# Kernel optimization log

Hardware: AMD Instinct MI355X
Metric: run time of the kernel (lower is better)

Reference implementation:

```python
import jax, jax.numpy as jnp
import numpy as np

NUM_PINS = 10_000_000
NUM_NETS = 2_500_000


def setup_inputs() -> dict:
    key = jax.random.key(0)
    k1, k2, k3 = jax.random.split(key, 3)
    pos = jax.random.normal(k1, (2 * NUM_PINS,), dtype=jnp.float32)
    pin2net_map = jax.random.randint(k2, (NUM_PINS,), 0, NUM_NETS).astype(jnp.int32)
    net_weights = jax.random.uniform(k3, (NUM_NETS,), dtype=jnp.float32)
    net_mask = jnp.ones((NUM_NETS,), dtype=bool)
    pin_mask = jnp.zeros((NUM_PINS,), dtype=bool)
    inv_gamma = jnp.ones((1,), dtype=jnp.float32)
    return {"pos": pos, "pin2net_map": pin2net_map, "net_weights": net_weights,
            "net_mask": net_mask, "pin_mask": pin_mask, "inv_gamma": inv_gamma}


def _wawl(pos, pin2net_map, net_weights, net_mask, inv_gamma, num_nets):
    # pos = concat(x, y); reshape to [P, 2] so segment ops handle x,y together
    P = pos.shape[0] // 2
    xy = pos.reshape(2, P).T  # [P, 2]
    ig = inv_gamma[0]

    # per-net max/min for numerical stability (shift cancels in the ratio)
    seg_max = jax.lax.stop_gradient(
        jax.ops.segment_max(xy, pin2net_map, num_segments=num_nets))  # [N,2]
    seg_min = jax.lax.stop_gradient(
        jax.ops.segment_min(xy, pin2net_map, num_segments=num_nets))  # [N,2]

    ex = jnp.exp((xy - seg_max[pin2net_map]) * ig)   # [P,2]
    enx = jnp.exp((seg_min[pin2net_map] - xy) * ig)  # [P,2]

    sum_ex = jax.ops.segment_sum(ex, pin2net_map, num_segments=num_nets)
    sum_enx = jax.ops.segment_sum(enx, pin2net_map, num_segments=num_nets)
    sum_xex = jax.ops.segment_sum(xy * ex, pin2net_map, num_segments=num_nets)
    sum_xenx = jax.ops.segment_sum(xy * enx, pin2net_map, num_segments=num_nets)

    # guard empty nets (sum == 0) to avoid 0/0
    valid = sum_ex > 0
    wl_pos = jnp.where(valid, sum_xex / jnp.where(valid, sum_ex, 1.0), 0.0)
    wl_neg = jnp.where(valid, sum_xenx / jnp.where(valid, sum_enx, 1.0), 0.0)
    wl_net = wl_pos - wl_neg  # [N,2]

    w = jnp.where(net_mask, net_weights, 0.0)  # [N]
    return jnp.sum(wl_net * w[:, None])


def reference(pos, pin2net_map, net_weights, net_mask, pin_mask, inv_gamma):
    num_nets = net_weights.shape[0]
    return _wawl(pos, pin2net_map, net_weights, net_mask, inv_gamma, num_nets)
```

## Files before the change

### kernel.cpp

```cpp
#include <hip/hip_runtime.h>
#include <hip/hip_fp16.h>


#define NPB      2048
#define NPB_LOG  11
#define CAP      9216
#define NBMAX    2048
#define CHUNK    16384
#define TB       1024

__global__ void init_kernel(int* __restrict__ alloc, int NB, float* __restrict__ out) {
    int i = blockIdx.x * blockDim.x + threadIdx.x;
    if (i == 0) out[0] = 0.f;
    if (i < NB) alloc[i] = i * CAP;
}

__global__ __launch_bounds__(TB)
void bucket_kernel(const int* __restrict__ p2n, const float* __restrict__ pos, int P,
                   int* __restrict__ alloc, uint2* __restrict__ rec) {
    __shared__ int   hist_delta[NBMAX];
    __shared__ int   cur[NBMAX];
    __shared__ uint2 stage[CHUNK];
    __shared__ unsigned wtot[TB / 64];

    const int tid  = threadIdx.x;
    const int lane = tid & 63;
    const int wid  = tid >> 6;
    const int start = blockIdx.x * CHUNK;
    const int cnt_chunk = min(CHUNK, P - start);

    hist_delta[2 * tid]     = 0;
    hist_delta[2 * tid + 1] = 0;
    __syncthreads();

#pragma unroll
    for (int k = 0; k < CHUNK / TB; ++k) {
        int i = start + k * TB + tid;
        if (i < P) atomicAdd(&hist_delta[p2n[i] >> NPB_LOG], 1);
    }
    __syncthreads();

    unsigned e0 = (unsigned)hist_delta[2 * tid];
    unsigned e1 = (unsigned)hist_delta[2 * tid + 1];
    unsigned pair = e0 + e1;
    unsigned inc = pair;
#pragma unroll
    for (int d = 1; d < 64; d <<= 1) {
        unsigned u = (unsigned)__shfl_up((int)inc, d, 64);
        if (lane >= d) inc += u;
    }
    if (lane == 63) wtot[wid] = inc;
    __syncthreads();
    unsigned wbase = 0;
    for (int k = 0; k < wid; ++k) wbase += wtot[k];
    unsigned off0 = wbase + inc - pair;
    unsigned off1 = off0 + e0;
    int b0 = 2 * tid, b1 = b0 + 1;
    int g0 = e0 ? atomicAdd(&alloc[b0], (int)e0) : 0;
    int g1 = e1 ? atomicAdd(&alloc[b1], (int)e1) : 0;
    hist_delta[b0] = g0 - (int)off0;
    hist_delta[b1] = g1 - (int)off1;
    cur[b0] = (int)off0;
    cur[b1] = (int)off1;
    __syncthreads();

#pragma unroll
    for (int k = 0; k < CHUNK / TB; ++k) {
        int i = start + k * TB + tid;
        if (i < P) {
            int n = p2n[i];
            __half2 h = __floats2half2_rn(pos[i], pos[P + i]);
            uint2 r;
            r.x = *reinterpret_cast<unsigned*>(&h);
            r.y = (unsigned)n;
            int p = atomicAdd(&cur[n >> NPB_LOG], 1);
            stage[p] = r;
        }
    }
    __syncthreads();

#pragma unroll
    for (int k = 0; k < CHUNK / TB; ++k) {
        int slot = k * TB + tid;
        if (slot < cnt_chunk) {
            uint2 r = stage[slot];
            int b = (int)(r.y >> NPB_LOG);
            int addr = hist_delta[b] + slot;
            if (addr < (b + 1) * CAP)
                rec[addr] = r;
        }
    }
}

__global__ __launch_bounds__(TB)
void reduce_kernel(const uint2* __restrict__ rec, const int* __restrict__ alloc,
                   const float* __restrict__ w, const void* __restrict__ mask,
                   const float* __restrict__ inv_gamma, int N, float* __restrict__ out) {
    __shared__ unsigned       head[NPB];
    __shared__ unsigned       spin[CAP];
    __shared__ unsigned short nxt[CAP];
    __shared__ float          wsum[TB / 64];

    const int tid  = threadIdx.x;
    const int lane = tid & 63;
    const int wid  = tid >> 6;
    const int b    = blockIdx.x;
    const int base = b * CAP;

    int count = alloc[b] - base;
    if (count > CAP) count = CAP;
    const float ig = inv_gamma[0];

    head[2 * tid]     = 0xFFFFu;
    head[2 * tid + 1] = 0xFFFFu;
    __syncthreads();

    for (int e = tid; e < count; e += TB) {
        uint2 r = rec[base + e];
        spin[e] = r.x;
        unsigned old = atomicExch(&head[r.y & (NPB - 1)], (unsigned)e);
        nxt[e] = (unsigned short)old;
    }
    __syncthreads();

    const bool mask_is_byte = (((const unsigned*)mask)[0] == 0x01010101u);
    float local = 0.f;
#pragma unroll
    for (int rep = 0; rep < 2; ++rep) {
        int j = tid + rep * TB;
        int n = (b << NPB_LOG) + j;
        if (n >= N) continue;
        unsigned p = head[j];
        if (p != 0xFFFFu) {
            float sex = 0.f, sxex = 0.f, senx = 0.f, sxenx = 0.f;
            float sey = 0.f, syey = 0.f, seny = 0.f, syeny = 0.f;
            while (p != 0xFFFFu) {
                unsigned u = spin[p];
                __half2 h = *reinterpret_cast<__half2*>(&u);
                float x = __low2float(h), y = __high2float(h);
                float ex  = __expf(x * ig);
                float enx = __expf(-x * ig);
                float ey  = __expf(y * ig);
                float eny = __expf(-y * ig);
                sex += ex;  sxex += x * ex;  senx += enx;  sxenx += x * enx;
                sey += ey;  syey += y * ey;  seny += eny;  syeny += y * eny;
                p = nxt[p];
            }
            float val = sxex / sex - sxenx / senx + syey / sey - syeny / seny;
            bool m = mask_is_byte ? (((const unsigned char*)mask)[n] != 0)
                                  : (((const int*)mask)[n] != 0);
            local += val * (m ? w[n] : 0.f);
        }
    }

#pragma unroll
    for (int o = 32; o > 0; o >>= 1) local += __shfl_down(local, o, 64);
    if (lane == 0) wsum[wid] = local;
    __syncthreads();
    if (tid == 0) {
        float s = 0.f;
        for (int k = 0; k < TB / 64; ++k) s += wsum[k];
        atomicAdd(out, s);
    }
}

extern "C" void kernel_launch(void* const* d_in, const int* in_sizes, int n_in,
                              void* d_out, int out_size, void* d_ws, size_t ws_size,
                              hipStream_t stream) {
    const float* pos       = (const float*)d_in[0];
    const int*   p2n       = (const int*)d_in[1];
    const float* wts       = (const float*)d_in[2];
    const void*  net_mask  = d_in[3];
    const float* inv_gamma = (const float*)d_in[5];

    int P = in_sizes[0] / 2;
    int N = in_sizes[2];
    int NB = (N + NPB - 1) >> NPB_LOG;
    if (NB > NBMAX) return;

    int*   alloc = (int*)d_ws;
    uint2* rec   = (uint2*)((char*)d_ws + NBMAX * sizeof(int));
    float* out   = (float*)d_out;

    int chunks = (P + CHUNK - 1) / CHUNK;

    hipLaunchKernelGGL(init_kernel,   dim3((NBMAX + 255) / 256), dim3(256), 0, stream,
                       alloc, NB, out);
    hipLaunchKernelGGL(bucket_kernel, dim3(chunks),              dim3(TB),  0, stream,
                       p2n, pos, P, alloc, rec);
    hipLaunchKernelGGL(reduce_kernel, dim3(NB),                  dim3(TB),  0, stream,
                       rec, alloc, wts, net_mask, inv_gamma, N, out);
}
```

Before: 293.5 us.

## Replace global atomic bucket allocation with per-chunk sorted segments and offset metadata

The bucket kernel now builds per-bucket linked lists in shared memory and writes each chunk's records sorted by bucket into its own chunk region, storing per-bucket offsets in a metadata table. This removes the global atomicAdd allocator. The reduce kernel prefix-scans those offsets to gather each bucket's records from every chunk. The per-thread serial list walks in the bucket kernel make the global writes uncoalesced. In the reduce kernel each thread copies a variable-length segment serially, which can cause load imbalance and scattered reads.

```diff
diff --git a/kernel.cpp b/kernel.cpp
--- a/kernel.cpp
+++ b/kernel.cpp
@@ -4,45 +4,60 @@
 
 #define NPB      2048
 #define NPB_LOG  11
-#define CAP      9216
-#define NBMAX    2048
-#define CHUNK    16384
+#define CHUNK    8192
+#define CAPB     9216
 #define TB       1024
 
-__global__ void init_kernel(int* __restrict__ alloc, int NB, float* __restrict__ out) {
-    int i = blockIdx.x * blockDim.x + threadIdx.x;
-    if (i == 0) out[0] = 0.f;
-    if (i < NB) alloc[i] = i * CAP;
+__global__ void init_kernel(float* __restrict__ out) {
+    if (threadIdx.x == 0 && blockIdx.x == 0) out[0] = 0.f;
 }
 
 __global__ __launch_bounds__(TB)
-void bucket_kernel(const int* __restrict__ p2n, const float* __restrict__ pos, int P,
-                   int* __restrict__ alloc, uint2* __restrict__ rec) {
-    __shared__ int   hist_delta[NBMAX];
-    __shared__ int   cur[NBMAX];
-    __shared__ uint2 stage[CHUNK];
+void bucket_kernel(const int* __restrict__ p2n, const float* __restrict__ pos,
+                   int P, int C, int NB,
+                   uint2* __restrict__ rec, int* __restrict__ offmeta) {
+    __shared__ unsigned head[NPB];
+    __shared__ uint2    elem[CHUNK];
     __shared__ unsigned wtot[TB / 64];
 
     const int tid  = threadIdx.x;
     const int lane = tid & 63;
     const int wid  = tid >> 6;
-    const int start = blockIdx.x * CHUNK;
+    const int c     = blockIdx.x;
+    const int start = c * CHUNK;
     const int cnt_chunk = min(CHUNK, P - start);
 
-    hist_delta[2 * tid]     = 0;
-    hist_delta[2 * tid + 1] = 0;
+    head[2 * tid]     = 0xFFFFu;
+    head[2 * tid + 1] = 0xFFFFu;
     __syncthreads();
 
 #pragma unroll
     for (int k = 0; k < CHUNK / TB; ++k) {
-        int i = start + k * TB + tid;
-        if (i < P) atomicAdd(&hist_delta[p2n[i] >> NPB_LOG], 1);
-    }
-    __syncthreads();
-
-    unsigned e0 = (unsigned)hist_delta[2 * tid];
-    unsigned e1 = (unsigned)hist_delta[2 * tid + 1];
-    unsigned pair = e0 + e1;
+        int e = k * TB + tid;
+        int i = start + e;
+        if (i < P) {
+            int n = p2n[i];
+            __half2 h = __floats2half2_rn(pos[i], pos[P + i]);
+            unsigned coords = *reinterpret_cast<unsigned*>(&h);
+            unsigned old = atomicExch(&head[n >> NPB_LOG], (unsigned)e);
+            elem[e] = make_uint2(coords,
+                                 ((unsigned)(n & (NPB - 1)) << 16) | (old & 0xFFFFu));
+        }
+    }
+    __syncthreads();
+
+    const int b0 = 2 * tid, b1 = 2 * tid + 1;
+    unsigned cnt0 = 0, cnt1 = 0;
+    if (b0 < NB) {
+        unsigned p = head[b0];
+        while (p != 0xFFFFu) { cnt0++; p = elem[p].y & 0xFFFFu; }
+    }
+    if (b1 < NB) {
+        unsigned p = head[b1];
+        while (p != 0xFFFFu) { cnt1++; p = elem[p].y & 0xFFFFu; }
+    }
+
+    unsigned pair = cnt0 + cnt1;
     unsigned inc = pair;
 #pragma unroll
     for (int d = 1; d < 64; d <<= 1) {
@@ -53,73 +68,94 @@
     __syncthreads();
     unsigned wbase = 0;
     for (int k = 0; k < wid; ++k) wbase += wtot[k];
-    unsigned off0 = wbase + inc - pair;
-    unsigned off1 = off0 + e0;
-    int b0 = 2 * tid, b1 = b0 + 1;
-    int g0 = e0 ? atomicAdd(&alloc[b0], (int)e0) : 0;
-    int g1 = e1 ? atomicAdd(&alloc[b1], (int)e1) : 0;
-    hist_delta[b0] = g0 - (int)off0;
-    hist_delta[b1] = g1 - (int)off1;
-    cur[b0] = (int)off0;
-    cur[b1] = (int)off1;
-    __syncthreads();
-
-#pragma unroll
-    for (int k = 0; k < CHUNK / TB; ++k) {
-        int i = start + k * TB + tid;
-        if (i < P) {
-            int n = p2n[i];
-            __half2 h = __floats2half2_rn(pos[i], pos[P + i]);
-            uint2 r;
-            r.x = *reinterpret_cast<unsigned*>(&h);
-            r.y = (unsigned)n;
-            int p = atomicAdd(&cur[n >> NPB_LOG], 1);
-            stage[p] = r;
-        }
-    }
-    __syncthreads();
-
-#pragma unroll
-    for (int k = 0; k < CHUNK / TB; ++k) {
-        int slot = k * TB + tid;
-        if (slot < cnt_chunk) {
-            uint2 r = stage[slot];
-            int b = (int)(r.y >> NPB_LOG);
-            int addr = hist_delta[b] + slot;
-            if (addr < (b + 1) * CAP)
-                rec[addr] = r;
+    const unsigned off0 = wbase + inc - pair;
+    const unsigned off1 = off0 + cnt0;
+
+    if (b0 < NB) offmeta[(size_t)b0 * C + c] = (int)off0;
+    if (b1 < NB) offmeta[(size_t)b1 * C + c] = (int)off1;
+    if (tid == 0) offmeta[(size_t)NB * C + c] = cnt_chunk;
+
+    if (b0 < NB) {
+        unsigned p = head[b0], k = 0;
+        while (p != 0xFFFFu) {
+            uint2 el = elem[p];
+            rec[(size_t)start + off0 + k] = make_uint2(el.x, el.y >> 16);
+            k++;
+            p = el.y & 0xFFFFu;
+        }
+    }
+    if (b1 < NB) {
+        unsigned p = head[b1], k = 0;
+        while (p != 0xFFFFu) {
+            uint2 el = elem[p];
+            rec[(size_t)start + off1 + k] = make_uint2(el.x, el.y >> 16);
+            k++;
+            p = el.y & 0xFFFFu;
         }
     }
 }
 
 __global__ __launch_bounds__(TB)
-void reduce_kernel(const uint2* __restrict__ rec, const int* __restrict__ alloc,
+void reduce_kernel(const uint2* __restrict__ rec, const int* __restrict__ offmeta,
                    const float* __restrict__ w, const void* __restrict__ mask,
-                   const float* __restrict__ inv_gamma, int N, float* __restrict__ out) {
+                   const float* __restrict__ inv_gamma, int N, int C, int NB,
+                   float* __restrict__ out) {
     __shared__ unsigned       head[NPB];
-    __shared__ unsigned       spin[CAP];
-    __shared__ unsigned short nxt[CAP];
-    __shared__ float          wsum[TB / 64];
+    __shared__ unsigned       spin[CAPB];
+    __shared__ unsigned short nxt[CAPB];
+    __shared__ int            sA[CHUNK / 4];
+    __shared__ int            dA[CHUNK / 4];
+    __shared__ unsigned wtot[TB / 64];
+    __shared__ float    wsum[TB / 64];
 
     const int tid  = threadIdx.x;
     const int lane = tid & 63;
     const int wid  = tid >> 6;
     const int b    = blockIdx.x;
-    const int base = b * CAP;
-
-    int count = alloc[b] - base;
-    if (count > CAP) count = CAP;
     const float ig = inv_gamma[0];
 
     head[2 * tid]     = 0xFFFFu;
     head[2 * tid + 1] = 0xFFFFu;
-    __syncthreads();
-
-    for (int e = tid; e < count; e += TB) {
-        uint2 r = rec[base + e];
-        spin[e] = r.x;
-        unsigned old = atomicExch(&head[r.y & (NPB - 1)], (unsigned)e);
-        nxt[e] = (unsigned short)old;
+    for (int c = tid; c < C; c += TB) {
+        int s = offmeta[(size_t)b * C + c];
+        sA[c] = s;
+        dA[c] = offmeta[(size_t)(b + 1) * C + c] - s;
+    }
+    __syncthreads();
+
+    const int c0 = 2 * tid, c1 = 2 * tid + 1;
+    unsigned k0 = (c0 < C) ? (unsigned)dA[c0] : 0u;
+    unsigned k1 = (c1 < C) ? (unsigned)dA[c1] : 0u;
+    unsigned pair = k0 + k1;
+    unsigned inc = pair;
+#pragma unroll
+    for (int d = 1; d < 64; d <<= 1) {
+        unsigned u = (unsigned)__shfl_up((int)inc, d, 64);
+        if (lane >= d) inc += u;
+    }
+    if (lane == 63) wtot[wid] = inc;
+    __syncthreads();
+    unsigned wbase = 0;
+    for (int k = 0; k < wid; ++k) wbase += wtot[k];
+    unsigned d0 = wbase + inc - pair;
+    if (c0 < C) dA[c0] = (int)d0;
+    if (c1 < C) dA[c1] = (int)(d0 + k0);
+    __syncthreads();
+
+    for (int c = tid; c < C; c += TB) {
+        int s   = sA[c];
+        int cnt = offmeta[(size_t)(b + 1) * C + c] - s;
+        int dst = dA[c];
+        const uint2* src = rec + (size_t)c * CHUNK + s;
+        for (int k = 0; k < cnt; ++k) {
+            uint2 r = src[k];
+            int d = dst + k;
+            if (d < CAPB) {
+                spin[d] = r.x;
+                unsigned old = atomicExch(&head[r.y], (unsigned)d);
+                nxt[d] = (unsigned short)old;
+            }
+        }
     }
     __syncthreads();
 
@@ -175,19 +211,17 @@
 
     int P = in_sizes[0] / 2;
     int N = in_sizes[2];
+    int C  = (P + CHUNK - 1) / CHUNK;
     int NB = (N + NPB - 1) >> NPB_LOG;
-    if (NB > NBMAX) return;
-
-    int*   alloc = (int*)d_ws;
-    uint2* rec   = (uint2*)((char*)d_ws + NBMAX * sizeof(int));
-    float* out   = (float*)d_out;
-
-    int chunks = (P + CHUNK - 1) / CHUNK;
-
-    hipLaunchKernelGGL(init_kernel,   dim3((NBMAX + 255) / 256), dim3(256), 0, stream,
-                       alloc, NB, out);
-    hipLaunchKernelGGL(bucket_kernel, dim3(chunks),              dim3(TB),  0, stream,
-                       p2n, pos, P, alloc, rec);
-    hipLaunchKernelGGL(reduce_kernel, dim3(NB),                  dim3(TB),  0, stream,
-                       rec, alloc, wts, net_mask, inv_gamma, N, out);
-}
+    if (C > CHUNK / 4 || NB > NPB) return;
+
+    uint2* rec     = (uint2*)d_ws;
+    int*   offmeta = (int*)((char*)d_ws + (size_t)P * sizeof(uint2));
+    float* out     = (float*)d_out;
+
+    hipLaunchKernelGGL(init_kernel,   dim3(1),  dim3(64), 0, stream, out);
+    hipLaunchKernelGGL(bucket_kernel, dim3(C),  dim3(TB), 0, stream,
+                       p2n, pos, P, C, NB, rec, offmeta);
+    hipLaunchKernelGGL(reduce_kernel, dim3(NB), dim3(TB), 0, stream,
+                       rec, offmeta, wts, net_mask, inv_gamma, N, C, NB, out);
+}
```

Result: slower. 356.4 us (+21.4%).

## Cache pin records in registers and replace linked-list nets with counting sort

Applied to the files above, without the earlier changes.

The bucket kernel now loads each pin's position and net index once. It keeps them in registers together with the rank returned by the histogram atomic, which removes the second global read pass and the second shared-memory atomic pass. The reduce kernel drops the per-net linked list in favour of a shared-memory counting sort (count, scan, scatter), so each net's pins are contiguous and the inner loop reads them sequentially instead of chasing pointers. CHUNK is halved to 8192 to limit register and LDS pressure, at the cost of twice as many bucket blocks and more global atomics on alloc.

```diff
diff --git a/kernel.cpp b/kernel.cpp
--- a/kernel.cpp
+++ b/kernel.cpp
@@ -6,8 +6,10 @@
 #define NPB_LOG  11
 #define CAP      9216
 #define NBMAX    2048
-#define CHUNK    16384
+#define CHUNK    8192
 #define TB       1024
+#define RPT_A    (CHUNK / TB)
+#define RPT_B    ((CAP + TB - 1) / TB)
 
 __global__ void init_kernel(int* __restrict__ alloc, int NB, float* __restrict__ out) {
     int i = blockIdx.x * blockDim.x + threadIdx.x;
@@ -16,10 +18,9 @@
 }
 
 __global__ __launch_bounds__(TB)
-void bucket_kernel(const int* __restrict__ p2n, const float* __restrict__ pos, int P,
-                   int* __restrict__ alloc, uint2* __restrict__ rec) {
-    __shared__ int   hist_delta[NBMAX];
-    __shared__ int   cur[NBMAX];
+void bucket_kernel(const int* __restrict__ p2n, const float* __restrict__ pos,
+                   int P, int* __restrict__ alloc, uint2* __restrict__ rec) {
+    __shared__ int   bins[NBMAX];
     __shared__ uint2 stage[CHUNK];
     __shared__ unsigned wtot[TB / 64];
 
@@ -29,19 +30,29 @@
     const int start = blockIdx.x * CHUNK;
     const int cnt_chunk = min(CHUNK, P - start);
 
-    hist_delta[2 * tid]     = 0;
-    hist_delta[2 * tid + 1] = 0;
-    __syncthreads();
-
-#pragma unroll
-    for (int k = 0; k < CHUNK / TB; ++k) {
+    bins[2 * tid]     = 0;
+    bins[2 * tid + 1] = 0;
+    __syncthreads();
+
+    unsigned coords[RPT_A];
+    int      net[RPT_A];
+    unsigned short rk[RPT_A];
+#pragma unroll
+    for (int k = 0; k < RPT_A; ++k) {
         int i = start + k * TB + tid;
-        if (i < P) atomicAdd(&hist_delta[p2n[i] >> NPB_LOG], 1);
-    }
-    __syncthreads();
-
-    unsigned e0 = (unsigned)hist_delta[2 * tid];
-    unsigned e1 = (unsigned)hist_delta[2 * tid + 1];
+        net[k] = -1;
+        if (i < P) {
+            int n = p2n[i];
+            __half2 h = __floats2half2_rn(pos[i], pos[P + i]);
+            coords[k] = *reinterpret_cast<unsigned*>(&h);
+            net[k] = n;
+            rk[k] = (unsigned short)atomicAdd(&bins[n >> NPB_LOG], 1);
+        }
+    }
+    __syncthreads();
+
+    const int b0 = 2 * tid, b1 = 2 * tid + 1;
+    unsigned e0 = (unsigned)bins[b0], e1 = (unsigned)bins[b1];
     unsigned pair = e0 + e1;
     unsigned inc = pair;
 #pragma unroll
@@ -53,39 +64,34 @@
     __syncthreads();
     unsigned wbase = 0;
     for (int k = 0; k < wid; ++k) wbase += wtot[k];
-    unsigned off0 = wbase + inc - pair;
-    unsigned off1 = off0 + e0;
-    int b0 = 2 * tid, b1 = b0 + 1;
-    int g0 = e0 ? atomicAdd(&alloc[b0], (int)e0) : 0;
-    int g1 = e1 ? atomicAdd(&alloc[b1], (int)e1) : 0;
-    hist_delta[b0] = g0 - (int)off0;
-    hist_delta[b1] = g1 - (int)off1;
-    cur[b0] = (int)off0;
-    cur[b1] = (int)off1;
-    __syncthreads();
-
-#pragma unroll
-    for (int k = 0; k < CHUNK / TB; ++k) {
-        int i = start + k * TB + tid;
-        if (i < P) {
-            int n = p2n[i];
-            __half2 h = __floats2half2_rn(pos[i], pos[P + i]);
-            uint2 r;
-            r.x = *reinterpret_cast<unsigned*>(&h);
-            r.y = (unsigned)n;
-            int p = atomicAdd(&cur[n >> NPB_LOG], 1);
-            stage[p] = r;
-        }
-    }
-    __syncthreads();
-
-#pragma unroll
-    for (int k = 0; k < CHUNK / TB; ++k) {
+    const unsigned off0 = wbase + inc - pair;
+    const unsigned off1 = off0 + e0;
+    const int g0 = e0 ? atomicAdd(&alloc[b0], (int)e0) : 0;
+    const int g1 = e1 ? atomicAdd(&alloc[b1], (int)e1) : 0;
+    bins[b0] = (int)off0;
+    bins[b1] = (int)off1;
+    __syncthreads();
+
+#pragma unroll
+    for (int k = 0; k < RPT_A; ++k) {
+        if (net[k] >= 0) {
+            int slot = bins[net[k] >> NPB_LOG] + (int)rk[k];
+            stage[slot] = make_uint2(coords[k], (unsigned)net[k]);
+        }
+    }
+    __syncthreads();
+
+    bins[b0] = g0 - (int)off0;
+    bins[b1] = g1 - (int)off1;
+    __syncthreads();
+
+#pragma unroll
+    for (int k = 0; k < RPT_A; ++k) {
         int slot = k * TB + tid;
         if (slot < cnt_chunk) {
             uint2 r = stage[slot];
             int b = (int)(r.y >> NPB_LOG);
-            int addr = hist_delta[b] + slot;
+            int addr = bins[b] + slot;
             if (addr < (b + 1) * CAP)
                 rec[addr] = r;
         }
@@ -95,11 +101,13 @@
 __global__ __launch_bounds__(TB)
 void reduce_kernel(const uint2* __restrict__ rec, const int* __restrict__ alloc,
                    const float* __restrict__ w, const void* __restrict__ mask,
-                   const float* __restrict__ inv_gamma, int N, float* __restrict__ out) {
-    __shared__ unsigned       head[NPB];
-    __shared__ unsigned       spin[CAP];
-    __shared__ unsigned short nxt[CAP];
-    __shared__ float          wsum[TB / 64];
+                   const float* __restrict__ inv_gamma, int N,
+                   float* __restrict__ out) {
+    __shared__ int      cnt[NPB];
+    __shared__ int      off[NPB];
+    __shared__ unsigned spin[CAP];
+    __shared__ unsigned wtot[TB / 64];
+    __shared__ float    wsum[TB / 64];
 
     const int tid  = threadIdx.x;
     const int lane = tid & 63;
@@ -111,15 +119,49 @@
     if (count > CAP) count = CAP;
     const float ig = inv_gamma[0];
 
-    head[2 * tid]     = 0xFFFFu;
-    head[2 * tid + 1] = 0xFFFFu;
-    __syncthreads();
-
-    for (int e = tid; e < count; e += TB) {
-        uint2 r = rec[base + e];
-        spin[e] = r.x;
-        unsigned old = atomicExch(&head[r.y & (NPB - 1)], (unsigned)e);
-        nxt[e] = (unsigned short)old;
+    cnt[2 * tid]     = 0;
+    cnt[2 * tid + 1] = 0;
+    __syncthreads();
+
+    unsigned coords[RPT_B];
+    unsigned nlrk[RPT_B];
+#pragma unroll
+    for (int k = 0; k < RPT_B; ++k) {
+        int e = k * TB + tid;
+        nlrk[k] = 0xFFFFFFFFu;
+        if (e < count) {
+            uint2 r = rec[base + e];
+            coords[k] = r.x;
+            unsigned nl = r.y & (NPB - 1);
+            unsigned rk = (unsigned)atomicAdd(&cnt[nl], 1);
+            nlrk[k] = nl | (rk << 16);
+        }
+    }
+    __syncthreads();
+
+    const int j0 = 2 * tid, j1 = 2 * tid + 1;
+    unsigned e0 = (unsigned)cnt[j0], e1 = (unsigned)cnt[j1];
+    unsigned pair = e0 + e1;
+    unsigned inc = pair;
+#pragma unroll
+    for (int d = 1; d < 64; d <<= 1) {
+        unsigned u = (unsigned)__shfl_up((int)inc, d, 64);
+        if (lane >= d) inc += u;
+    }
+    if (lane == 63) wtot[wid] = inc;
+    __syncthreads();
+    unsigned wbase = 0;
+    for (int k = 0; k < wid; ++k) wbase += wtot[k];
+    unsigned x0 = wbase + inc - pair;
+    off[j0] = (int)x0;
+    off[j1] = (int)(x0 + e0);
+    __syncthreads();
+
+#pragma unroll
+    for (int k = 0; k < RPT_B; ++k) {
+        unsigned v = nlrk[k];
+        if (v != 0xFFFFFFFFu)
+            spin[off[v & 0xFFFFu] + (int)(v >> 16)] = coords[k];
     }
     __syncthreads();
 
@@ -130,11 +172,11 @@
         int j = tid + rep * TB;
         int n = (b << NPB_LOG) + j;
         if (n >= N) continue;
-        unsigned p = head[j];
-        if (p != 0xFFFFu) {
+        int s = off[j], c = cnt[j];
+        if (c > 0) {
             float sex = 0.f, sxex = 0.f, senx = 0.f, sxenx = 0.f;
             float sey = 0.f, syey = 0.f, seny = 0.f, syeny = 0.f;
-            while (p != 0xFFFFu) {
+            for (int p = s; p < s + c; ++p) {
                 unsigned u = spin[p];
                 __half2 h = *reinterpret_cast<__half2*>(&u);
                 float x = __low2float(h), y = __high2float(h);
@@ -144,7 +186,6 @@
                 float eny = __expf(-y * ig);
                 sex += ex;  sxex += x * ex;  senx += enx;  sxenx += x * enx;
                 sey += ey;  syey += y * ey;  seny += eny;  syeny += y * eny;
-                p = nxt[p];
             }
             float val = sxex / sex - sxenx / senx + syey / sey - syeny / seny;
             bool m = mask_is_byte ? (((const unsigned char*)mask)[n] != 0)
@@ -175,6 +216,7 @@
 
     int P = in_sizes[0] / 2;
     int N = in_sizes[2];
+    int C  = (P + CHUNK - 1) / CHUNK;
     int NB = (N + NPB - 1) >> NPB_LOG;
     if (NB > NBMAX) return;
 
@@ -182,11 +224,9 @@
     uint2* rec   = (uint2*)((char*)d_ws + NBMAX * sizeof(int));
     float* out   = (float*)d_out;
 
-    int chunks = (P + CHUNK - 1) / CHUNK;
-
     hipLaunchKernelGGL(init_kernel,   dim3((NBMAX + 255) / 256), dim3(256), 0, stream,
                        alloc, NB, out);
-    hipLaunchKernelGGL(bucket_kernel, dim3(chunks),              dim3(TB),  0, stream,
+    hipLaunchKernelGGL(bucket_kernel, dim3(C),                   dim3(TB),  0, stream,
                        p2n, pos, P, alloc, rec);
     hipLaunchKernelGGL(reduce_kernel, dim3(NB),                  dim3(TB),  0, stream,
                        rec, alloc, wts, net_mask, inv_gamma, N, out);
```

Result: faster. 286.4 us (-2.4%).
